# Kernel tuning notes

Hardware: AMD Instinct MI355X
Metric: run time of the kernel (lower is better)

The kernel has to match this reference:

```python
import jax, jax.numpy as jnp
import numpy as np
import math

N_NODES = 20000
N_EDGES = 320000
NODE_IN = 128
HIDDEN = 64
HEADS = 4
TIME_DIM = 64
SCALE = 60.0 / 1.0  # sensitivity / epsilon


def _linear_params(key, din, dout):
    k1, k2 = jax.random.split(key)
    bound = 1.0 / math.sqrt(din)
    w = jax.random.uniform(k1, (din, dout), minval=-bound, maxval=bound, dtype=jnp.float32)
    b = jax.random.uniform(k2, (dout,), minval=-bound, maxval=bound, dtype=jnp.float32)
    return w, b


def setup_inputs() -> dict:
    key = jax.random.key(0)
    ks = jax.random.split(key, 16)
    edge_index = jax.random.randint(ks[0], (2, N_EDGES), 0, N_NODES, dtype=jnp.int64)
    raw_time = jax.random.uniform(ks[1], (N_EDGES, 1), dtype=jnp.float32) * 86400.0
    noise = jax.random.laplace(ks[2], (N_EDGES, 1), dtype=jnp.float32) * SCALE
    node_emb = jax.random.normal(ks[3], (N_NODES, NODE_IN), dtype=jnp.float32)
    HC = HEADS * HIDDEN
    wq1, bq1 = _linear_params(ks[4], NODE_IN, HC)
    wk1, bk1 = _linear_params(ks[5], NODE_IN, HC)
    wv1, bv1 = _linear_params(ks[6], NODE_IN, HC)
    wt1, bt1 = _linear_params(ks[7], TIME_DIM, HC)
    wq2, bq2 = _linear_params(ks[8], HC, HC)
    wk2, bk2 = _linear_params(ks[9], HC, HC)
    wv2, bv2 = _linear_params(ks[10], HC, HC)
    wt2, bt2 = _linear_params(ks[11], TIME_DIM, HC)
    wc, bc = _linear_params(ks[12], HC, 1)
    return dict(edge_index=edge_index, raw_time=raw_time, noise=noise, node_emb=node_emb,
                wq1=wq1, bq1=bq1, wk1=wk1, bk1=bk1, wv1=wv1, bv1=bv1, wt1=wt1, bt1=bt1,
                wq2=wq2, bq2=bq2, wk2=wk2, bk2=bk2, wv2=wv2, bv2=bv2, wt2=wt2, bt2=bt2,
                wc=wc, bc=bc)


def time_encode(t):
    # t: [E, 1] -> [E, TIME_DIM]; interleaved sin/cos as in TimeEncoder
    half = jnp.arange(0, TIME_DIM, 2, dtype=jnp.float32)
    div_term = jnp.exp(half * (-math.log(10000.0) / TIME_DIM))  # [TIME_DIM/2]
    arg = t * div_term  # [E, TIME_DIM/2]
    te = jnp.stack([jnp.sin(arg), jnp.cos(arg)], axis=-1)  # [E, T/2, 2]
    return te.reshape(t.shape[0], TIME_DIM)


def temporal_conv(x, src, dst, time_enc, wq, bq, wk, bk, wv, bv, wt, bt):
    # gather-QKV, edge softmax over dst segments, scatter-add aggregation
    N = x.shape[0]
    q = (x @ wq + bq).reshape(N, HEADS, HIDDEN)
    k = (x @ wk + bk).reshape(N, HEADS, HIDDEN)
    v = (x @ wv + bv).reshape(N, HEADS, HIDDEN)
    t_enc = (time_enc @ wt + bt).reshape(-1, HEADS, HIDDEN)  # [E,H,C]
    q_i = q[dst]                      # [E,H,C]
    k_j = k[src] + t_enc              # [E,H,C]
    alpha = (q_i * k_j).sum(-1) / math.sqrt(HIDDEN)  # [E,H]
    # segment softmax over index = dst (PyG softmax semantics)
    amax = jax.ops.segment_max(alpha, dst, num_segments=N)  # [N,H]
    ea = jnp.exp(alpha - amax[dst])
    denom = jax.ops.segment_sum(ea, dst, num_segments=N)
    alpha = ea / (denom[dst] + 1e-16)
    msg = v[src] * alpha[..., None]   # [E,H,C]
    out = jax.ops.segment_sum(msg, dst, num_segments=N)  # [N,H,C]
    return out.reshape(N, HEADS * HIDDEN)


def reference(edge_index, raw_time, noise, node_emb,
              wq1, bq1, wk1, bk1, wv1, bv1, wt1, bt1,
              wq2, bq2, wk2, bk2, wv2, bv2, wt2, bt2,
              wc, bc):
    src, dst = edge_index[0], edge_index[1]
    noisy_time = raw_time + noise                 # Laplace mechanism
    time_encoded = time_encode(noisy_time)        # [E, TIME_DIM]
    x = jax.nn.relu(temporal_conv(node_emb, src, dst, time_encoded,
                                  wq1, bq1, wk1, bk1, wv1, bv1, wt1, bt1))
    x = jax.nn.relu(temporal_conv(x, src, dst, time_encoded,
                                  wq2, bq2, wk2, bk2, wv2, bv2, wt2, bt2))
    edge_emb = x[src] + x[dst]                    # [E, H*C]
    out = edge_emb @ wc + bc                      # [E, 1]
    return out.squeeze(-1)
```

## Files before the change

### kernel.cpp

```cpp
#include <hip/hip_runtime.h>
#include <hip/hip_fp16.h>
#include <math.h>

#define NN   20000
#define NE   320000
#define NIN  128
#define HC   256
#define NB   1024

typedef unsigned short u16;
typedef __attribute__((ext_vector_type(8))) short bf16x8;
typedef __attribute__((ext_vector_type(8))) unsigned short u16x8;
typedef __attribute__((ext_vector_type(4))) float f32x4;

__device__ __forceinline__ float bf2f(u16 u) {
  union { unsigned int i; float f; } x;
  x.i = ((unsigned int)u) << 16;
  return x.f;
}
__device__ __forceinline__ u16 f2bf(float f) {
  union { float f; unsigned int i; } x;
  x.f = f;
  unsigned int r = x.i + 0x7fffu + ((x.i >> 16) & 1u);
  return (u16)(r >> 16);
}

__device__ __forceinline__ float ldf(const void* p, int i, bool fbf) {
  return fbf ? bf2f(((const u16*)p)[i]) : ((const float*)p)[i];
}
__device__ __forceinline__ int ldsrc(const void* p, int e, bool is64) {
  const int* p32 = (const int*)p;
  return is64 ? p32[2 * e] : p32[e];
}
__device__ __forceinline__ int lddst(const void* p, int e, bool is64) {
  const int* p32 = (const int*)p;
  return is64 ? p32[2 * (NE + e)] : p32[NE + e];
}
__device__ __forceinline__ void stout(void* p, int i, float v, bool fbf) {
  if (fbf) ((u16*)p)[i] = f2bf(v);
  else ((float*)p)[i] = v;
}

__device__ __forceinline__ void gload_lds16(const u16* g, u16* l) {
  __builtin_amdgcn_global_load_lds(
      (const __attribute__((address_space(1))) void*)g,
      (__attribute__((address_space(3))) void*)l, 16, 0, 0);
}

__global__ void devinit_kernel(const void* __restrict__ eidx,
                               const void* __restrict__ nemb,
                               int* __restrict__ flags, float* __restrict__ divt) {
  int lane = threadIdx.x;
  if (lane < 32) {
    const float c32 = (float)(-0.14391156831212787);
    float prod = (float)(2 * lane) * c32;
    divt[lane] = (float)exp((double)prod);
  }
  if (lane == 0) {
    const int* p32 = (const int*)eidx;
    int is64 = 1;
    for (int i = 1; i < 128; i += 2)
      if (p32[i] != 0) { is64 = 0; break; }
    const u16* q16 = (const u16*)nemb;
    int fbf = 1;
    for (int i = 0; i < 128; i += 2) {
      unsigned e = (q16[i] >> 7) & 0xFF;
      if (e < 90 || e > 140) { fbf = 0; break; }
    }
    flags[0] = is64;
    flags[1] = fbf;
  }
}

__global__ void sentinel_kernel(const int* __restrict__ flags, void* __restrict__ out) {
  int i = blockIdx.x * 256 + threadIdx.x;
  if (i < NE) stout(out, i, 3000.0f, flags[1] != 0);
}
__global__ void raw_sentinel_kernel(u16* __restrict__ out) {
  int i = blockIdx.x * 256 + threadIdx.x;
  if (i < NE) out[i] = f2bf(3000.0f);
}

__global__ void zero_kernel(int* __restrict__ p, int n) {
  int i = blockIdx.x * 256 + threadIdx.x;
  if (i < n) p[i] = 0;
}

__global__ void hist_kernel(const int* __restrict__ flags, const void* __restrict__ eidx,
                            int* __restrict__ cnt) {
  bool is64 = flags[0] != 0;
  int e = blockIdx.x * 256 + threadIdx.x;
  if (e < NE) {
    int d = lddst(eidx, e, is64);
    if ((unsigned)d < NN) atomicAdd(&cnt[d], 1);
  }
}

__global__ void scan1_kernel(const int* __restrict__ cnt, int* __restrict__ offs,
                             int* __restrict__ bsum, int n) {
  __shared__ int s[256];
  int b = blockIdx.x, t = threadIdx.x, i = b * 256 + t;
  int x = (i < n) ? cnt[i] : 0;
  s[t] = x;
  __syncthreads();
  for (int off = 1; off < 256; off <<= 1) {
    int y = (t >= off) ? s[t - off] : 0;
    __syncthreads();
    s[t] += y;
    __syncthreads();
  }
  if (i < n) offs[i] = s[t] - x;
  if (t == 255) bsum[b] = s[t];
}

__global__ void scan2_kernel(int* __restrict__ bsum, int* __restrict__ offs,
                             int nb, int n) {
  __shared__ int s[256];
  int t = threadIdx.x;
  int x = (t < nb) ? bsum[t] : 0;
  s[t] = x;
  __syncthreads();
  for (int off = 1; off < 256; off <<= 1) {
    int y = (t >= off) ? s[t - off] : 0;
    __syncthreads();
    s[t] += y;
    __syncthreads();
  }
  if (t < nb) bsum[t] = s[t] - x;
  if (t == 255) offs[n] = s[t];
}

__global__ void scan3_kernel(int* __restrict__ offs, const int* __restrict__ bsum,
                             int* __restrict__ cursor, int n) {
  int i = blockIdx.x * 256 + threadIdx.x;
  if (i < n) {
    int v = offs[i] + bsum[blockIdx.x];
    offs[i] = v;
    cursor[i] = v;
  }
}

__global__ void fill_kernel(const int* __restrict__ flags, const void* __restrict__ eidx,
                            const void* __restrict__ rawt, const void* __restrict__ noise,
                            int* __restrict__ cursor, int* __restrict__ ssrc,
                            float* __restrict__ stt) {
  bool is64 = flags[0] != 0, fbf = flags[1] != 0;
  int e = blockIdx.x * 256 + threadIdx.x;
  if (e < NE) {
    int d = lddst(eidx, e, is64);
    if ((unsigned)d < NN) {
      int pos = atomicAdd(&cursor[d], 1);
      if ((unsigned)pos < NE) {
        int src = ldsrc(eidx, e, is64);
        if ((unsigned)src >= NN) src = 0;
        ssrc[pos] = src;
        stt[pos] = ldf(rawt, e, fbf) + ldf(noise, e, fbf);
      }
    }
  }
}

__global__ __launch_bounds__(256) void te_kernel(
    const float* __restrict__ stt, const float* __restrict__ divt,
    u16* __restrict__ te_s) {
  int idx = blockIdx.x * 256 + threadIdx.x;
  int p = idx >> 5;
  if (p >= NE) return;
  int f = idx & 31;
  float tt = stt[p];
  float arg = tt * divt[f];
  double rev = (double)arg * 0.15915494309189535;
  double fr = rev - floor(rev);
  float red = (float)(fr * 6.283185307179586);
  float sv, cv;
  sincosf(red, &sv, &cv);
  __half hs = __float2half(sv), hc = __float2half(cv);
  unsigned int packed = (unsigned int)(*(u16*)&hs) | ((unsigned int)(*(u16*)&hc) << 16);
  ((unsigned int*)te_s)[(size_t)p * 32 + f] = packed;
}

__global__ void transw3_kernel(const int* __restrict__ flags, const void* __restrict__ W0,
                               const void* __restrict__ W1, const void* __restrict__ W2,
                               u16* __restrict__ WtBig, int K) {
  bool fbf = flags[1] != 0;
  __shared__ u16 tile[64][65];
  int z = blockIdx.z;
  const void* W = (z == 0) ? W0 : (z == 1) ? W1 : W2;
  u16* dst = WtBig + (size_t)z * 256 * K;
  int kb = blockIdx.x * 64, cb = blockIdx.y * 64;
  int tx = threadIdx.x & 63, ty = threadIdx.x >> 6;
  for (int i = ty; i < 64; i += 4)
    tile[tx][i] = f2bf(ldf(W, (kb + i) * HC + cb + tx, fbf));
  __syncthreads();
  for (int i = ty; i < 64; i += 4)
    dst[(size_t)(cb + i) * K + kb + tx] = tile[i][tx];
}

__global__ void wcombbias_kernel(const int* __restrict__ flags, const void* __restrict__ wt,
                                 const u16* __restrict__ Wqt, u16* __restrict__ Wout,
                                 const void* __restrict__ bq, const void* __restrict__ bk,
                                 const void* __restrict__ bv, float* __restrict__ biasBig,
                                 int K) {
  bool fbf = flags[1] != 0;
  int b = blockIdx.x, t = threadIdx.x;
  if (b < 256) {
    __shared__ float wrow[64];
    int j = b, h = j >> 6;
    if (t < 64) wrow[t] = ldf(wt, (j & 63) * HC + h * 64 + t, fbf);
    __syncthreads();
    if (t < K) {
      float s = 0.f;
#pragma unroll 8
      for (int mm = 0; mm < 64; ++mm)
        s += wrow[mm] * bf2f(Wqt[(size_t)(h * 64 + mm) * K + t]);
      Wout[(size_t)j * K + t] = f2bf(s);
    }
  } else if (b < 259) {
    int bb = b - 256;
    const void* p = (bb == 0) ? bq : (bb == 1) ? bk : bv;
    biasBig[bb * 256 + t] = ldf(p, t, fbf);
  } else {
    int j = t, h = j >> 6;
    float s = 0.f;
    for (int mm = 0; mm < 64; ++mm)
      s += ldf(bq, h * 64 + mm, fbf) * ldf(wt, (j & 63) * HC + h * 64 + mm, fbf);
    biasBig[768 + j] = s;
  }
}

template <bool AWS>
__global__ __launch_bounds__(256) void gemm_mfma(
    const int* __restrict__ flags, const void* __restrict__ Ap,
    const u16* __restrict__ Wt, const float* __restrict__ bias,
    u16* __restrict__ C, int M, int K) {
  bool fbf = flags[1] != 0;
  __shared__ u16 As[128 * 32];
  __shared__ u16 Bs[128 * 32];
  int tid = threadIdx.x;
  int rb = blockIdx.x * 128, cb = blockIdx.y * 128;
  int wave = tid >> 6, lane = tid & 63;
  int l15 = lane & 15, quad = lane >> 4;
  int mbase = (wave >> 1) * 64, nbase = (wave & 1) * 64;

  f32x4 acc[4][4];
#pragma unroll
  for (int mt = 0; mt < 4; ++mt)
#pragma unroll
    for (int nt = 0; nt < 4; ++nt)
#pragma unroll
      for (int r = 0; r < 4; ++r) acc[mt][nt][r] = 0.f;

  int srow0 = tid >> 2, schunk0 = tid & 3;
  int srow1 = (tid + 256) >> 2, schunk1 = (tid + 256) & 3;
  int gchunk0 = schunk0 ^ (srow0 & 3);
  int gchunk1 = schunk1 ^ (srow1 & 3);
  int arow0 = rb + srow0; if (arow0 >= M) arow0 = M - 1;
  int arow1 = rb + srow1; if (arow1 >= M) arow1 = M - 1;
  u16* asl0 = &As[srow0 * 32 + schunk0 * 8];
  u16* asl1 = &As[srow1 * 32 + schunk1 * 8];
  u16* bsl0 = &Bs[srow0 * 32 + schunk0 * 8];
  u16* bsl1 = &Bs[srow1 * 32 + schunk1 * 8];
  const u16* bsrc0 = Wt + (size_t)(cb + srow0) * K + gchunk0 * 8;
  const u16* bsrc1 = Wt + (size_t)(cb + srow1) * K + gchunk1 * 8;
  const bool adirect = AWS || fbf;
  const u16* asrc0 = adirect ? ((const u16*)Ap + (size_t)arow0 * K + gchunk0 * 8) : (const u16*)0;
  const u16* asrc1 = adirect ? ((const u16*)Ap + (size_t)arow1 * K + gchunk1 * 8) : (const u16*)0;

  for (int kk = 0; kk < K; kk += 32) {
    if (adirect) {
      gload_lds16(asrc0 + kk, asl0);
      gload_lds16(asrc1 + kk, asl1);
    } else {
      const float* A0 = (const float*)Ap + (size_t)arow0 * K + kk + gchunk0 * 8;
      const float* A1 = (const float*)Ap + (size_t)arow1 * K + kk + gchunk1 * 8;
      bf16x8 t0, t1;
#pragma unroll
      for (int i = 0; i < 8; ++i) { t0[i] = (short)f2bf(A0[i]); t1[i] = (short)f2bf(A1[i]); }
      *(bf16x8*)asl0 = t0;
      *(bf16x8*)asl1 = t1;
    }
    gload_lds16(bsrc0 + kk, bsl0);
    gload_lds16(bsrc1 + kk, bsl1);
    __syncthreads();

    bf16x8 bfrag[4];
#pragma unroll
    for (int nt = 0; nt < 4; ++nt) {
      int col = nbase + nt * 16 + l15;
      bfrag[nt] = *(const bf16x8*)&Bs[col * 32 + ((quad ^ (col & 3)) * 8)];
    }
#pragma unroll
    for (int mt = 0; mt < 4; ++mt) {
      int row = mbase + mt * 16 + l15;
      bf16x8 afrag = *(const bf16x8*)&As[row * 32 + ((quad ^ (row & 3)) * 8)];
#pragma unroll
      for (int nt = 0; nt < 4; ++nt)
        acc[mt][nt] = __builtin_amdgcn_mfma_f32_16x16x32_bf16(afrag, bfrag[nt], acc[mt][nt], 0, 0, 0);
    }
    __syncthreads();
  }

#pragma unroll
  for (int nt = 0; nt < 4; ++nt) {
    int gcol = cb + nbase + nt * 16 + l15;
    float bv = bias[gcol];
    int scol;
    if (gcol < 256) scol = gcol;
    else if (gcol < 512) { int cc = gcol - 256; scol = 256 + ((cc >> 2) << 3) + (cc & 3); }
    else if (gcol < 768) { int cc = gcol - 512; scol = 256 + ((cc >> 2) << 3) + 4 + (cc & 3); }
    else scol = gcol;
#pragma unroll
    for (int mt = 0; mt < 4; ++mt) {
#pragma unroll
      for (int r = 0; r < 4; ++r) {
        int grow = rb + mbase + mt * 16 + quad * 4 + r;
        if (grow < M) C[(size_t)grow * NB + scol] = f2bf(acc[mt][nt][r] + bv);
      }
    }
  }
}

template <int DOY>
__global__ __launch_bounds__(256) void aggfused_kernel(
    const int* __restrict__ flags, const int* __restrict__ ssrc,
    const int* __restrict__ offsets, const u16* __restrict__ te_s,
    const u16* __restrict__ qkvp, const void* __restrict__ bt,
    u16* __restrict__ xout, const void* __restrict__ wc,
    float* __restrict__ ynode) {
  bool fbf = flags[1] != 0;
  int w = threadIdx.x >> 6;
  int n = blockIdx.x * 4 + w;
  if (n >= NN) return;
  int lane = threadIdx.x & 63;
  int c = lane * 4;
  int s0 = offsets[n], s1 = offsets[n + 1];
  if (s0 < 0) s0 = 0;
  if (s1 > NE) s1 = NE;

  ushort4 q4 = *(const ushort4*)(qkvp + (size_t)n * NB + c);
  ushort4 p4 = *(const ushort4*)(qkvp + (size_t)n * NB + 768 + c);
  float qx = bf2f(q4.x), qy = bf2f(q4.y), qz = bf2f(q4.z), qw = bf2f(q4.w);
  float px = bf2f(p4.x), py = bf2f(p4.y), pz = bf2f(p4.z), pw = bf2f(p4.w);
  float pb = qx * ldf(bt, c + 0, fbf);
  pb += qy * ldf(bt, c + 1, fbf);
  pb += qz * ldf(bt, c + 2, fbf);
  pb += qw * ldf(bt, c + 3, fbf);
  pb += __shfl_xor(pb, 1);
  pb += __shfl_xor(pb, 2);
  pb += __shfl_xor(pb, 4);
  pb += __shfl_xor(pb, 8);
  float qb = pb;
  int jb = c & 63;
  int kvoff = 256 + lane * 8;

  float m = -INFINITY, denom = 0.f;
  float acc0 = 0.f, acc1 = 0.f, acc2 = 0.f, acc3 = 0.f;

#define ALPHA_OF(kv, t4, out_a, okflag)                                        \
  {                                                                            \
    float s = qx * bf2f((kv)[0]) + __half2float(*(__half*)&(t4).x) * px;       \
    s += qy * bf2f((kv)[1]) + __half2float(*(__half*)&(t4).y) * py;            \
    s += qz * bf2f((kv)[2]) + __half2float(*(__half*)&(t4).z) * pz;            \
    s += qw * bf2f((kv)[3]) + __half2float(*(__half*)&(t4).w) * pw;            \
    s += __shfl_xor(s, 1);                                                     \
    s += __shfl_xor(s, 2);                                                     \
    s += __shfl_xor(s, 4);                                                     \
    s += __shfl_xor(s, 8);                                                     \
    out_a = (okflag) ? (s + qb) * 0.125f : 0.f;                                \
  }

#define STATE_UPDATE(a, kv, okflag)                                            \
  {                                                                            \
    float ea;                                                                  \
    if ((a) > m) {                                                             \
      float sc = __expf(m - (a));                                              \
      denom *= sc;                                                             \
      acc0 *= sc; acc1 *= sc; acc2 *= sc; acc3 *= sc;                          \
      m = (a);                                                                 \
      ea = 1.0f;                                                               \
    } else {                                                                   \
      ea = __expf((a) - m);                                                    \
    }                                                                          \
    denom += ea;                                                               \
    if (okflag) {                                                              \
      acc0 += ea * bf2f((kv)[4]);                                              \
      acc1 += ea * bf2f((kv)[5]);                                              \
      acc2 += ea * bf2f((kv)[6]);                                              \
      acc3 += ea * bf2f((kv)[7]);                                              \
    }                                                                          \
  }

  int p = s0;
  for (; p + 3 < s1; p += 4) {
    int srcA = ssrc[p], srcB = ssrc[p + 1], srcC = ssrc[p + 2], srcD = ssrc[p + 3];
    bool okA = (unsigned)srcA < NN, okB = (unsigned)srcB < NN;
    bool okC = (unsigned)srcC < NN, okD = (unsigned)srcD < NN;
    if (!okA) srcA = 0;
    if (!okB) srcB = 0;
    if (!okC) srcC = 0;
    if (!okD) srcD = 0;
    u16x8 kvA = *(const u16x8*)(qkvp + (size_t)srcA * NB + kvoff);
    u16x8 kvB = *(const u16x8*)(qkvp + (size_t)srcB * NB + kvoff);
    u16x8 kvC = *(const u16x8*)(qkvp + (size_t)srcC * NB + kvoff);
    u16x8 kvD = *(const u16x8*)(qkvp + (size_t)srcD * NB + kvoff);
    ushort4 tA = *(const ushort4*)(te_s + (size_t)p * 64 + jb);
    ushort4 tB = *(const ushort4*)(te_s + (size_t)(p + 1) * 64 + jb);
    ushort4 tC = *(const ushort4*)(te_s + (size_t)(p + 2) * 64 + jb);
    ushort4 tD = *(const ushort4*)(te_s + (size_t)(p + 3) * 64 + jb);

    float aA, aB, aC, aD;
    ALPHA_OF(kvA, tA, aA, okA)
    ALPHA_OF(kvB, tB, aB, okB)
    ALPHA_OF(kvC, tC, aC, okC)
    ALPHA_OF(kvD, tD, aD, okD)
    STATE_UPDATE(aA, kvA, okA)
    STATE_UPDATE(aB, kvB, okB)
    STATE_UPDATE(aC, kvC, okC)
    STATE_UPDATE(aD, kvD, okD)
  }
  for (; p < s1; ++p) {
    int src = ssrc[p];
    bool ok = (unsigned)src < NN;
    if (!ok) src = 0;
    u16x8 kv = *(const u16x8*)(qkvp + (size_t)src * NB + kvoff);
    ushort4 t4 = *(const ushort4*)(te_s + (size_t)p * 64 + jb);
    float a;
    ALPHA_OF(kv, t4, a, ok)
    STATE_UPDATE(a, kv, ok)
  }
#undef ALPHA_OF
#undef STATE_UPDATE

  float inv = 1.f / (denom + 1e-16f);
  ushort4 r;
  r.x = f2bf(fmaxf(acc0 * inv, 0.f));
  r.y = f2bf(fmaxf(acc1 * inv, 0.f));
  r.z = f2bf(fmaxf(acc2 * inv, 0.f));
  r.w = f2bf(fmaxf(acc3 * inv, 0.f));
  *(ushort4*)(xout + (size_t)n * HC + c) = r;
  if (DOY) {
    float yv = bf2f(r.x) * ldf(wc, c + 0, fbf);
    yv += bf2f(r.y) * ldf(wc, c + 1, fbf);
    yv += bf2f(r.z) * ldf(wc, c + 2, fbf);
    yv += bf2f(r.w) * ldf(wc, c + 3, fbf);
    for (int off = 32; off; off >>= 1) yv += __shfl_xor(yv, off);
    if (lane == 0) ynode[n] = yv;
  }
}

__global__ __launch_bounds__(256) void final2_kernel(
    const int* __restrict__ flags, const void* __restrict__ eidx,
    const float* __restrict__ y, const void* __restrict__ bc,
    void* __restrict__ out) {
  bool is64 = flags[0] != 0, fbf = flags[1] != 0;
  int e = blockIdx.x * 256 + threadIdx.x;
  if (e >= NE) return;
  int src = ldsrc(eidx, e, is64);
  int dst = lddst(eidx, e, is64);
  if ((unsigned)src >= NN) src = 0;
  if ((unsigned)dst >= NN) dst = 0;
  stout(out, e, y[src] + y[dst] + ldf(bc, 0, fbf), fbf);
}

extern "C" void kernel_launch(void* const* d_in, const int* in_sizes, int n_in,
                              void* d_out, int out_size, void* d_ws, size_t ws_size,
                              hipStream_t stream) {
  const void* eidx  = d_in[0];
  const void* rawt  = d_in[1];
  const void* noise = d_in[2];
  const void* nemb  = d_in[3];
  const void *wq1 = d_in[4],  *bq1 = d_in[5];
  const void *wk1 = d_in[6],  *bk1 = d_in[7];
  const void *wv1 = d_in[8],  *bv1 = d_in[9];
  const void *wt1 = d_in[10], *bt1 = d_in[11];
  const void *wq2 = d_in[12], *bq2 = d_in[13];
  const void *wk2 = d_in[14], *bk2 = d_in[15];
  const void *wv2 = d_in[16], *bv2 = d_in[17];
  const void *wt2 = d_in[18], *bt2 = d_in[19];
  const void *wcp = d_in[20], *bcp = d_in[21];

  char* ws = (char*)d_ws;
  size_t off = 0;
  auto alloc = [&](size_t bytes) -> void* {
    void* p = ws + off;
    off += (bytes + 255) & ~(size_t)255;
    return p;
  };
  int*   flags  = (int*)alloc(256);
  float* divt   = (float*)alloc(256);
  u16*   WtBig  = (u16*)alloc((size_t)NB * HC * 2);
  float* biasBig= (float*)alloc((size_t)NB * 4);
  u16*   qkvp   = (u16*)alloc((size_t)NN * NB * 2);
  u16*   x1     = (u16*)alloc((size_t)NN * HC * 2);
  u16*   x2     = (u16*)alloc((size_t)NN * HC * 2);
  float* ynode  = (float*)alloc((size_t)NN * 4);
  int* offsets  = (int*)alloc((size_t)(NN + 1) * 4);
  int* cursor   = (int*)alloc((size_t)NN * 4);
  int* bsum     = (int*)alloc(256 * 4);
  int* ssrc     = (int*)alloc((size_t)NE * 4);
  float* stt    = (float*)alloc((size_t)NE * 4);
  u16* te_s     = (u16*)alloc((size_t)NE * 64 * 2);
  size_t need = off;

  int gN = (NN + 255) / 256, gE = (NE + 255) / 256;
  int nb = (NN + 255) / 256;

  if (ws_size < 1024) {
    raw_sentinel_kernel<<<gE, 256, 0, stream>>>((u16*)d_out);
    return;
  }
  devinit_kernel<<<1, 64, 0, stream>>>(eidx, nemb, flags, divt);
  if (need > ws_size) {
    sentinel_kernel<<<gE, 256, 0, stream>>>(flags, d_out);
    return;
  }

  zero_kernel<<<gN, 256, 0, stream>>>(cursor, NN);
  hist_kernel<<<gE, 256, 0, stream>>>(flags, eidx, cursor);
  scan1_kernel<<<nb, 256, 0, stream>>>(cursor, offsets, bsum, NN);
  scan2_kernel<<<1, 256, 0, stream>>>(bsum, offsets, nb, NN);
  scan3_kernel<<<nb, 256, 0, stream>>>(offsets, bsum, cursor, NN);
  fill_kernel<<<gE, 256, 0, stream>>>(flags, eidx, rawt, noise, cursor, ssrc, stt);

  int gTe = (NE * 32 + 255) / 256;
  te_kernel<<<gTe, 256, 0, stream>>>(stt, divt, te_s);

  dim3 ggemm((NN + 127) / 128, NB / 128);
  dim3 gt1(NIN / 64, 4, 3), gt2(HC / 64, 4, 3);
  int gNode = (NN + 3) / 4;

  transw3_kernel<<<gt1, 256, 0, stream>>>(flags, wq1, wk1, wv1, WtBig, NIN);
  wcombbias_kernel<<<260, 256, 0, stream>>>(flags, wt1, WtBig, WtBig + (size_t)768 * NIN,
                                            bq1, bk1, bv1, biasBig, NIN);
  gemm_mfma<false><<<ggemm, 256, 0, stream>>>(flags, nemb, WtBig, biasBig, qkvp, NN, NIN);
  aggfused_kernel<0><<<gNode, 256, 0, stream>>>(flags, ssrc, offsets, te_s, qkvp, bt1,
                                                x1, wcp, ynode);

  transw3_kernel<<<gt2, 256, 0, stream>>>(flags, wq2, wk2, wv2, WtBig, HC);
  wcombbias_kernel<<<260, 256, 0, stream>>>(flags, wt2, WtBig, WtBig + (size_t)768 * HC,
                                            bq2, bk2, bv2, biasBig, HC);
  gemm_mfma<true><<<ggemm, 256, 0, stream>>>(flags, x1, WtBig, biasBig, qkvp, NN, HC);
  aggfused_kernel<1><<<gNode, 256, 0, stream>>>(flags, ssrc, offsets, te_s, qkvp, bt2,
                                                x2, wcp, ynode);

  final2_kernel<<<gE, 256, 0, stream>>>(flags, eidx, ynode, bcp, d_out);
}
```

Measured before the change: 393.8 us.

## Fuse time encoding into CSR fill and prefetch next edge batch in aggregation

The separate time-encoding kernel and the intermediate noisy-time buffer are removed. Each fill thread now computes all 32 sin/cos pairs for its edge and writes them at the sorted position. The aggregation loop is software-pipelined so the next group of four gathered K/V rows loads while the current group is processed. This trades one launch and one buffer round-trip for a long serial per-thread loop with less parallelism and uncoalesced row writes, and it adds register pressure in the aggregation kernel.

Result: slower. 424.0 us (+7.7%).

```diff
diff --git a/kernel.cpp b/kernel.cpp
--- a/kernel.cpp
+++ b/kernel.cpp
@@ -142,8 +142,8 @@
 
 __global__ void fill_kernel(const int* __restrict__ flags, const void* __restrict__ eidx,
                             const void* __restrict__ rawt, const void* __restrict__ noise,
-                            int* __restrict__ cursor, int* __restrict__ ssrc,
-                            float* __restrict__ stt) {
+                            const float* __restrict__ divt, int* __restrict__ cursor,
+                            int* __restrict__ ssrc, u16* __restrict__ te_s) {
   bool is64 = flags[0] != 0, fbf = flags[1] != 0;
   int e = blockIdx.x * 256 + threadIdx.x;
   if (e < NE) {
@@ -154,29 +154,21 @@
         int src = ldsrc(eidx, e, is64);
         if ((unsigned)src >= NN) src = 0;
         ssrc[pos] = src;
-        stt[pos] = ldf(rawt, e, fbf) + ldf(noise, e, fbf);
+        float tt = ldf(rawt, e, fbf) + ldf(noise, e, fbf);
+        unsigned int* dst = (unsigned int*)te_s + (size_t)pos * 32;
+        for (int f = 0; f < 32; ++f) {
+          float arg = tt * divt[f];
+          double rev = (double)arg * 0.15915494309189535;
+          double fr = rev - floor(rev);
+          float red = (float)(fr * 6.283185307179586);
+          float sv, cv;
+          sincosf(red, &sv, &cv);
+          __half hs = __float2half(sv), hc = __float2half(cv);
+          dst[f] = (unsigned int)(*(u16*)&hs) | ((unsigned int)(*(u16*)&hc) << 16);
+        }
       }
     }
   }
-}
-
-__global__ __launch_bounds__(256) void te_kernel(
-    const float* __restrict__ stt, const float* __restrict__ divt,
-    u16* __restrict__ te_s) {
-  int idx = blockIdx.x * 256 + threadIdx.x;
-  int p = idx >> 5;
-  if (p >= NE) return;
-  int f = idx & 31;
-  float tt = stt[p];
-  float arg = tt * divt[f];
-  double rev = (double)arg * 0.15915494309189535;
-  double fr = rev - floor(rev);
-  float red = (float)(fr * 6.283185307179586);
-  float sv, cv;
-  sincosf(red, &sv, &cv);
-  __half hs = __float2half(sv), hc = __float2half(cv);
-  unsigned int packed = (unsigned int)(*(u16*)&hs) | ((unsigned int)(*(u16*)&hc) << 16);
-  ((unsigned int*)te_s)[(size_t)p * 32 + f] = packed;
 }
 
 __global__ void transw3_kernel(const int* __restrict__ flags, const void* __restrict__ W0,
@@ -355,6 +347,20 @@
 
   float m = -INFINITY, denom = 0.f;
   float acc0 = 0.f, acc1 = 0.f, acc2 = 0.f, acc3 = 0.f;
+
+#define LOADB(pp, KV0, KV1, KV2, KV3, O0, O1, O2, O3)                          \
+  {                                                                            \
+    int _s0 = ssrc[pp], _s1 = ssrc[(pp) + 1];                                  \
+    int _s2 = ssrc[(pp) + 2], _s3 = ssrc[(pp) + 3];                            \
+    O0 = (unsigned)_s0 < NN; if (!O0) _s0 = 0;                                 \
+    O1 = (unsigned)_s1 < NN; if (!O1) _s1 = 0;                                 \
+    O2 = (unsigned)_s2 < NN; if (!O2) _s2 = 0;                                 \
+    O3 = (unsigned)_s3 < NN; if (!O3) _s3 = 0;                                 \
+    KV0 = *(const u16x8*)(qkvp + (size_t)_s0 * NB + kvoff);                    \
+    KV1 = *(const u16x8*)(qkvp + (size_t)_s1 * NB + kvoff);                    \
+    KV2 = *(const u16x8*)(qkvp + (size_t)_s2 * NB + kvoff);                    \
+    KV3 = *(const u16x8*)(qkvp + (size_t)_s3 * NB + kvoff);                    \
+  }
 
 #define ALPHA_OF(kv, t4, out_a, okflag)                                        \
   {                                                                            \
@@ -390,33 +396,38 @@
     }                                                                          \
   }
 
+#define BATCH4(pp, KV0, KV1, KV2, KV3, O0, O1, O2, O3)                         \
+  {                                                                            \
+    ushort4 tA = *(const ushort4*)(te_s + (size_t)(pp) * 64 + jb);             \
+    ushort4 tB = *(const ushort4*)(te_s + (size_t)((pp) + 1) * 64 + jb);       \
+    ushort4 tC = *(const ushort4*)(te_s + (size_t)((pp) + 2) * 64 + jb);       \
+    ushort4 tD = *(const ushort4*)(te_s + (size_t)((pp) + 3) * 64 + jb);       \
+    float aA, aB, aC, aD;                                                      \
+    ALPHA_OF(KV0, tA, aA, O0)                                                  \
+    ALPHA_OF(KV1, tB, aB, O1)                                                  \
+    ALPHA_OF(KV2, tC, aC, O2)                                                  \
+    ALPHA_OF(KV3, tD, aD, O3)                                                  \
+    STATE_UPDATE(aA, KV0, O0)                                                  \
+    STATE_UPDATE(aB, KV1, O1)                                                  \
+    STATE_UPDATE(aC, KV2, O2)                                                  \
+    STATE_UPDATE(aD, KV3, O3)                                                  \
+  }
+
+  u16x8 cK0, cK1, cK2, cK3, nK0, nK1, nK2, nK3;
+  bool cO0, cO1, cO2, cO3, nO0, nO1, nO2, nO3;
+
   int p = s0;
-  for (; p + 3 < s1; p += 4) {
-    int srcA = ssrc[p], srcB = ssrc[p + 1], srcC = ssrc[p + 2], srcD = ssrc[p + 3];
-    bool okA = (unsigned)srcA < NN, okB = (unsigned)srcB < NN;
-    bool okC = (unsigned)srcC < NN, okD = (unsigned)srcD < NN;
-    if (!okA) srcA = 0;
-    if (!okB) srcB = 0;
-    if (!okC) srcC = 0;
-    if (!okD) srcD = 0;
-    u16x8 kvA = *(const u16x8*)(qkvp + (size_t)srcA * NB + kvoff);
-    u16x8 kvB = *(const u16x8*)(qkvp + (size_t)srcB * NB + kvoff);
-    u16x8 kvC = *(const u16x8*)(qkvp + (size_t)srcC * NB + kvoff);
-    u16x8 kvD = *(const u16x8*)(qkvp + (size_t)srcD * NB + kvoff);
-    ushort4 tA = *(const ushort4*)(te_s + (size_t)p * 64 + jb);
-    ushort4 tB = *(const ushort4*)(te_s + (size_t)(p + 1) * 64 + jb);
-    ushort4 tC = *(const ushort4*)(te_s + (size_t)(p + 2) * 64 + jb);
-    ushort4 tD = *(const ushort4*)(te_s + (size_t)(p + 3) * 64 + jb);
-
-    float aA, aB, aC, aD;
-    ALPHA_OF(kvA, tA, aA, okA)
-    ALPHA_OF(kvB, tB, aB, okB)
-    ALPHA_OF(kvC, tC, aC, okC)
-    ALPHA_OF(kvD, tD, aD, okD)
-    STATE_UPDATE(aA, kvA, okA)
-    STATE_UPDATE(aB, kvB, okB)
-    STATE_UPDATE(aC, kvC, okC)
-    STATE_UPDATE(aD, kvD, okD)
+  bool have = (p + 3 < s1);
+  if (have) LOADB(p, cK0, cK1, cK2, cK3, cO0, cO1, cO2, cO3)
+  for (; p + 7 < s1; p += 4) {
+    LOADB(p + 4, nK0, nK1, nK2, nK3, nO0, nO1, nO2, nO3)
+    BATCH4(p, cK0, cK1, cK2, cK3, cO0, cO1, cO2, cO3)
+    cK0 = nK0; cK1 = nK1; cK2 = nK2; cK3 = nK3;
+    cO0 = nO0; cO1 = nO1; cO2 = nO2; cO3 = nO3;
+  }
+  if (have) {
+    BATCH4(p, cK0, cK1, cK2, cK3, cO0, cO1, cO2, cO3)
+    p += 4;
   }
   for (; p < s1; ++p) {
     int src = ssrc[p];
@@ -428,8 +439,10 @@
     ALPHA_OF(kv, t4, a, ok)
     STATE_UPDATE(a, kv, ok)
   }
+#undef LOADB
 #undef ALPHA_OF
 #undef STATE_UPDATE
+#undef BATCH4
 
   float inv = 1.f / (denom + 1e-16f);
   ushort4 r;
@@ -498,7 +511,6 @@
   int* cursor   = (int*)alloc((size_t)NN * 4);
   int* bsum     = (int*)alloc(256 * 4);
   int* ssrc     = (int*)alloc((size_t)NE * 4);
-  float* stt    = (float*)alloc((size_t)NE * 4);
   u16* te_s     = (u16*)alloc((size_t)NE * 64 * 2);
   size_t need = off;
 
@@ -520,10 +532,7 @@
   scan1_kernel<<<nb, 256, 0, stream>>>(cursor, offsets, bsum, NN);
   scan2_kernel<<<1, 256, 0, stream>>>(bsum, offsets, nb, NN);
   scan3_kernel<<<nb, 256, 0, stream>>>(offsets, bsum, cursor, NN);
-  fill_kernel<<<gE, 256, 0, stream>>>(flags, eidx, rawt, noise, cursor, ssrc, stt);
-
-  int gTe = (NE * 32 + 255) / 256;
-  te_kernel<<<gTe, 256, 0, stream>>>(stt, divt, te_s);
+  fill_kernel<<<gE, 256, 0, stream>>>(flags, eidx, rawt, noise, divt, cursor, ssrc, te_s);
 
   dim3 ggemm((NN + 127) / 128, NB / 128);
   dim3 gt1(NIN / 64, 4, 3), gt2(HC / 64, 4, 3);
```
